# Kernel optimization log

Hardware: AMD Instinct MI355X
Metric: run time of the kernel (lower is better)

Reference implementation:

```python
import jax, jax.numpy as jnp
import numpy as np

B, C, CE, H, W = 4, 128, 64, 64, 64
V = H * W
# parent(i) < i//2 guarantees depth <= ceil(log2(V)) = 12; 14 is a safe static bound
MAX_LEVELS = 14


def _gather_v(x, idx):
    # x: [B, C, V], idx: [B, V] -> gather along vertex dim (broadcast over C)
    return jnp.take_along_axis(x, idx[:, None, :], axis=2)


def _tree_filter(feature_in, embed_in, sorted_index, sorted_parent, node_level):
    Bv, Cv, Hv, Wv = feature_in.shape
    Vv = Hv * Wv
    f = feature_in.reshape(Bv, Cv, Vv)
    e = embed_in.reshape(Bv, embed_in.shape[1], Vv)
    # build_edge_weight: gather to BFS order, gather parent, squared-L2 distance, exp(-d)
    f_s = _gather_v(f, sorted_index)          # [B,C,V] features in topological order
    e_s = _gather_v(e, sorted_index)
    e_p = _gather_v(e_s, sorted_parent)
    d2 = jnp.sum((e_s - e_p) ** 2, axis=1)    # [B,V]
    w = jnp.exp(-d2)                          # edge weight node->parent (root: exp(0)=1, unused)
    wB = w[:, None, :]
    # ---- up sweep (leaves -> root), level-parallel over BFS levels ----
    # A_i = f_i + sum_{c in child(i)} w_c * A_c ; Z_i = 1 + sum w_c * Z_c (self_weight = 1)
    aggr_up = f_s
    nrm_up = jnp.ones((Bv, Vv), feature_in.dtype)
    for d in range(MAX_LEVELS - 1, 0, -1):
        mw = jnp.where(node_level == d, w, jnp.zeros((), feature_in.dtype))
        aggr_up = jax.vmap(lambda a, p, m: a.at[:, p].add(m))(
            aggr_up, sorted_parent, mw[:, None, :] * aggr_up)
        nrm_up = jax.vmap(lambda a, p, m: a.at[p].add(m))(
            nrm_up, sorted_parent, mw * nrm_up)
    # ---- down sweep (root -> leaves) ----
    # Ahat_i = A_i + w_i * (Ahat_parent - w_i * A_i); root keeps A_root
    aggr = aggr_up
    nrm = nrm_up
    for d in range(1, MAX_LEVELS):
        sel = node_level == d
        pa = _gather_v(aggr, sorted_parent)
        aggr = jnp.where(sel[:, None, :], aggr_up + wB * (pa - wB * aggr_up), aggr)
        pn = jnp.take_along_axis(nrm, sorted_parent, axis=1)
        nrm = jnp.where(sel, nrm_up + w * (pn - w * nrm_up), nrm)
    out_s = aggr / nrm[:, None, :]
    # scatter back from BFS order to original vertex order
    out = jax.vmap(lambda o, i: jnp.zeros_like(o).at[:, i].set(o))(out_s, sorted_index)
    return out.reshape(Bv, Cv, Hv, Wv)


def setup_inputs() -> dict:
    key = jax.random.key(0)
    k1, k2 = jax.random.split(key)
    feature_in = jax.random.normal(k1, (B, C, H, W), dtype=jnp.float32)
    embed_in = 0.1 * jax.random.normal(k2, (B, CE, H, W), dtype=jnp.float32)
    rng = np.random.default_rng(0)
    sorted_index = np.stack([rng.permutation(V) for _ in range(B)]).astype(np.int32)
    sorted_parent = np.zeros((B, V), dtype=np.int32)
    node_level = np.zeros((B, V), dtype=np.int32)
    for b in range(B):
        for i in range(1, V):
            p = int(rng.integers(0, max(1, i // 2)))  # parent earlier in order, depth <= log2(V)
            sorted_parent[b, i] = p
            node_level[b, i] = node_level[b, p] + 1
    return {
        "feature_in": feature_in,
        "embed_in": embed_in,
        "sorted_index": jnp.asarray(sorted_index),
        "sorted_parent": jnp.asarray(sorted_parent),
        "node_level": jnp.asarray(node_level),
    }


def reference(feature_in, embed_in, sorted_index, sorted_parent, node_level):
    return _tree_filter(feature_in, embed_in, sorted_index, sorted_parent, node_level)
```

## Files before the change

### kernel.cpp

```cpp
#include <hip/hip_runtime.h>

#define BB 4
#define CC 128
#define CE 64
#define VV 4096
#define NLEV 14


__device__ __forceinline__ void lds_fadd(float* p, float v) {
    unsafeAtomicAdd(p, v);
}

__global__ __launch_bounds__(256) void prep_kernel(
    const float* __restrict__ embed,
    const int* __restrict__ sorted_index,
    const int* __restrict__ sorted_parent,
    const int* __restrict__ node_level,
    float* __restrict__ wsort,
    int*   __restrict__ giInv,
    int2*  __restrict__ cpl,
    int*   __restrict__ offs)
{
    int tid = threadIdx.x;
    if (blockIdx.x < BB) {
        int b = blockIdx.x;
        __shared__ int pos_s[VV];
        __shared__ int whist[4][16];
        __shared__ int cursor[NLEV];
        __shared__ int offSh[NLEV + 1];
        const int* lev = node_level    + b * VV;
        const int* si  = sorted_index  + b * VV;
        const int* par = sorted_parent + b * VV;
        int lane = tid & 63;
        int w    = tid >> 6;

        int dreg[16], sreg[16];
        int myc = 0;
        #pragma unroll
        for (int t = 0; t < 4; ++t) {
            int idx = tid + t * 256;
            int4 dv = ((const int4*)lev)[idx];
            int4 sv = ((const int4*)si)[idx];
            #pragma unroll
            for (int j = 0; j < 4; ++j) {
                int d = (&dv.x)[j]; d = d < NLEV - 1 ? d : NLEV - 1;
                dreg[t * 4 + j] = d;
                sreg[t * 4 + j] = (&sv.x)[j];
                #pragma unroll
                for (int dd = 0; dd < NLEV; ++dd) {
                    unsigned long long m = __ballot(d == dd);
                    myc += (lane == dd) ? (int)__popcll(m) : 0;
                }
            }
        }
        if (lane < 16) whist[w][lane] = myc;
        __syncthreads();
        if (tid == 0) {
            int acc = 0;
            for (int d = 0; d < NLEV; ++d) {
                int h = whist[0][d] + whist[1][d] + whist[2][d] + whist[3][d];
                offSh[d] = acc; cursor[d] = acc; acc += h;
            }
            offSh[NLEV] = acc;
        }
        __syncthreads();
        if (tid <= NLEV) offs[b * 16 + tid] = offSh[tid];

        int kreg[16];
        #pragma unroll
        for (int t = 0; t < 4; ++t) {
            #pragma unroll
            for (int j = 0; j < 4; ++j) {
                int i = 4 * (tid + t * 256) + j;
                int d = dreg[t * 4 + j];
                int k = 0;
                #pragma unroll
                for (int dd = 0; dd < NLEV; ++dd) {
                    unsigned long long m = __ballot(d == dd);
                    if (m) {
                        int leader = (int)__ffsll((unsigned long long)m) - 1;
                        int base = 0;
                        if (lane == leader) base = atomicAdd(&cursor[dd], (int)__popcll(m));
                        base = __shfl(base, leader, 64);
                        if (d == dd) k = base + (int)__popcll(m & ((1ull << lane) - 1ull));
                    }
                }
                kreg[t * 4 + j] = k;
                pos_s[i] = k;
                giInv[b * VV + sreg[t * 4 + j]] = k;
            }
        }
        __syncthreads();

        #pragma unroll
        for (int t = 0; t < 4; ++t) {
            int idx = tid + t * 256;
            int4 pv = ((const int4*)par)[idx];
            #pragma unroll
            for (int j = 0; j < 4; ++j) {
                int i = 4 * idx + j;
                int p = (&pv.x)[j];
                cpl[b * VV + kreg[t * 4 + j]] = make_int2(pos_s[p], i);
            }
        }
    } else {
        __shared__ float part[4][64];
        int bb   = blockIdx.x - BB;
        int b    = bb >> 6;
        int n0   = (bb & 63) << 6;
        int lane = tid & 63;
        int w    = tid >> 6;
        int i    = n0 + lane;
        int vi = sorted_index[b * VV + i];
        int p  = sorted_parent[b * VV + i];
        int vp = sorted_index[b * VV + p];
        const float* eb = embed + (size_t)b * CE * VV;
        float acc = 0.f;
        #pragma unroll
        for (int r = 0; r < 16; ++r) {
            int ce = w * 16 + r;
            float d = eb[ce * VV + vi] - eb[ce * VV + vp];
            acc = fmaf(d, d, acc);
        }
        part[w][lane] = acc;
        __syncthreads();
        if (w == 0) {
            float d2 = part[0][lane] + part[1][lane] + part[2][lane] + part[3][lane];
            wsort[b * VV + i] = __expf(-d2);
        }
    }
}

__global__ __launch_bounds__(512) void tree2_kernel(
    const float* __restrict__ feat,
    const float* __restrict__ wsort,
    const int*  __restrict__ giInv,
    const int2* __restrict__ cpl,
    const int*  __restrict__ offs,
    float* __restrict__ out)
{
    __shared__ float val0[VV];
    __shared__ float val1[VV];
    __shared__ float nrm[VV];
    __shared__ int   cw[VV];
    __shared__ int   offS[16];
    int b   = blockIdx.x >> 6;
    int c0  = (blockIdx.x & 63) << 1;
    int tid = threadIdx.x;

    const int2*  cplB = cpl   + b * VV;
    const int*   ivB  = giInv + b * VV;
    const float* wsB  = wsort + b * VV;
    const float* f0   = feat + ((size_t)(b * CC + c0)) * VV;
    const float* f1   = f0 + VV;

    if (tid < 16) offS[tid] = offs[b * 16 + tid];

    #pragma unroll
    for (int t = 0; t < 8; ++t) {
        int k = tid + t * 512;
        int2 x = cplB[k];
        int wb = __float_as_int(wsB[x.y]);
        cw[k] = (wb & 0xFFFFF000) | x.x;
    }

    int4 kkR[2];
    #pragma unroll
    for (int t = 0; t < 2; ++t) {
        int idx = tid + t * 512;
        int4   kk = ((const int4*)ivB)[idx];
        float4 a  = ((const float4*)f0)[idx];
        float4 bq = ((const float4*)f1)[idx];
        kkR[t] = kk;
        val0[kk.x] = a.x;  val0[kk.y] = a.y;  val0[kk.z] = a.z;  val0[kk.w] = a.w;
        val1[kk.x] = bq.x; val1[kk.y] = bq.y; val1[kk.z] = bq.z; val1[kk.w] = bq.w;
        nrm[kk.x] = 1.f;   nrm[kk.y] = 1.f;   nrm[kk.z] = 1.f;   nrm[kk.w] = 1.f;
    }
    __syncthreads();

    for (int d = NLEV - 1; d >= 1; --d) {
        int s = offS[d], e = offS[d + 1];
        if (s == e) continue;
        for (int k = s + tid; k < e; k += 512) {
            int x = cw[k];
            float w = __int_as_float(x & 0xFFFFF000);
            int  cp = x & 0xFFF;
            lds_fadd(&val0[cp], w * val0[k]);
            lds_fadd(&val1[cp], w * val1[k]);
            lds_fadd(&nrm[cp],  w * nrm[k]);
        }
        __syncthreads();
    }

    for (int d = 1; d <= NLEV - 1; ++d) {
        int s = offS[d], e = offS[d + 1];
        if (s == e) continue;
        for (int k = s + tid; k < e; k += 512) {
            int x = cw[k];
            float w = __int_as_float(x & 0xFFFFF000);
            int  cp = x & 0xFFF;
            float u0 = val0[k], u1 = val1[k], un = nrm[k];
            val0[k] = fmaf(w, fmaf(-w, u0, val0[cp]), u0);
            val1[k] = fmaf(w, fmaf(-w, u1, val1[cp]), u1);
            nrm[k]  = fmaf(w, fmaf(-w, un, nrm[cp]),  un);
        }
        __syncthreads();
    }

    float* o0 = out + ((size_t)(b * CC + c0)) * VV;
    float* o1 = o0 + VV;
    #pragma unroll
    for (int t = 0; t < 2; ++t) {
        int idx = tid + t * 512;
        int4 kk = kkR[t];
        float i0 = __fdividef(1.f, nrm[kk.x]);
        float i1 = __fdividef(1.f, nrm[kk.y]);
        float i2 = __fdividef(1.f, nrm[kk.z]);
        float i3 = __fdividef(1.f, nrm[kk.w]);
        float4 r0, r1;
        r0.x = val0[kk.x] * i0; r0.y = val0[kk.y] * i1;
        r0.z = val0[kk.z] * i2; r0.w = val0[kk.w] * i3;
        r1.x = val1[kk.x] * i0; r1.y = val1[kk.y] * i1;
        r1.z = val1[kk.z] * i2; r1.w = val1[kk.w] * i3;
        ((float4*)o0)[idx] = r0;
        ((float4*)o1)[idx] = r1;
    }
}

extern "C" void kernel_launch(void* const* d_in, const int* in_sizes, int n_in,
                              void* d_out, int out_size, void* d_ws, size_t ws_size,
                              hipStream_t stream) {
    const float* feat          = (const float*)d_in[0];
    const float* embed         = (const float*)d_in[1];
    const int*   sorted_index  = (const int*)d_in[2];
    const int*   sorted_parent = (const int*)d_in[3];
    const int*   node_level    = (const int*)d_in[4];
    float* out = (float*)d_out;

    char* ws = (char*)d_ws;
    const size_t A = (size_t)BB * VV * 4;
    float* wsort = (float*)(ws);
    int*   giInv = (int*)  (ws + A);
    int2*  cpl   = (int2*) (ws + 2 * A);
    int*   offs  = (int*)  (ws + 4 * A);

    prep_kernel<<<BB + BB * 64, 256, 0, stream>>>(
        embed, sorted_index, sorted_parent, node_level, wsort, giInv, cpl, offs);

    tree2_kernel<<<BB * CC / 2, 512, 0, stream>>>(
        feat, wsort, giInv, cpl, offs, out);
}
```

Baseline: 124.0 us.

## Replace ballot-based level bucketing with per-thread counts and LDS prefix scan

The per-batch sort of nodes by BFS level in the prep kernel now gives each thread a contiguous block of 16 vertices. Each thread counts and ranks them locally, and a shuffle-based exclusive scan over per-thread counts per level produces stable offsets. This replaces 14-way ballot loops and LDS atomics per element, cutting instruction count in the serial bucketing block. It adds a 14x256 int LDS table and changes global access to contiguous per-thread loads, which coalesce less well.

```diff
diff --git a/kernel.cpp b/kernel.cpp
--- a/kernel.cpp
+++ b/kernel.cpp
@@ -24,10 +24,11 @@
     int tid = threadIdx.x;
     if (blockIdx.x < BB) {
         int b = blockIdx.x;
-        __shared__ int pos_s[VV];
-        __shared__ int whist[4][16];
-        __shared__ int cursor[NLEV];
-        __shared__ int offSh[NLEV + 1];
+        __shared__ int  pos_s[VV];
+        __shared__ int4 cntv[NLEV * 64];
+        __shared__ int  tot[NLEV];
+        __shared__ int  offSh[NLEV + 1];
+        int* cnt = (int*)cntv;
         const int* lev = node_level    + b * VV;
         const int* si  = sorted_index  + b * VV;
         const int* par = sorted_parent + b * VV;
@@ -35,32 +36,59 @@
         int w    = tid >> 6;
 
         int dreg[16], sreg[16];
-        int myc = 0;
         #pragma unroll
         for (int t = 0; t < 4; ++t) {
-            int idx = tid + t * 256;
-            int4 dv = ((const int4*)lev)[idx];
-            int4 sv = ((const int4*)si)[idx];
+            int4 dv = ((const int4*)lev)[tid * 4 + t];
+            int4 sv = ((const int4*)si)[tid * 4 + t];
             #pragma unroll
             for (int j = 0; j < 4; ++j) {
                 int d = (&dv.x)[j]; d = d < NLEV - 1 ? d : NLEV - 1;
                 dreg[t * 4 + j] = d;
                 sreg[t * 4 + j] = (&sv.x)[j];
-                #pragma unroll
-                for (int dd = 0; dd < NLEV; ++dd) {
-                    unsigned long long m = __ballot(d == dd);
-                    myc += (lane == dd) ? (int)__popcll(m) : 0;
-                }
             }
         }
-        if (lane < 16) whist[w][lane] = myc;
+
+        int rank[16];
+        #pragma unroll
+        for (int m = 0; m < 16; ++m) {
+            int r = 0;
+            #pragma unroll
+            for (int m2 = 0; m2 < m; ++m2) r += (dreg[m2] == dreg[m]) ? 1 : 0;
+            rank[m] = r;
+        }
+
+        #pragma unroll
+        for (int d = 0; d < NLEV; ++d) {
+            int c = 0;
+            #pragma unroll
+            for (int m = 0; m < 16; ++m) c += (dreg[m] == d) ? 1 : 0;
+            cnt[d * 256 + tid] = c;
+        }
+        __syncthreads();
+
+        for (int d = w; d < NLEV; d += 4) {
+            int base = d * 64 + lane;
+            int4 cv = cntv[base];
+            int ls = cv.x + cv.y + cv.z + cv.w;
+            int x = ls;
+            #pragma unroll
+            for (int off = 1; off < 64; off <<= 1) {
+                int y = __shfl_up(x, off, 64);
+                if (lane >= off) x += y;
+            }
+            int excl = x - ls;
+            int4 ov;
+            ov.x = excl;
+            ov.y = excl + cv.x;
+            ov.z = excl + cv.x + cv.y;
+            ov.w = excl + cv.x + cv.y + cv.z;
+            cntv[base] = ov;
+            if (lane == 63) tot[d] = x;
+        }
         __syncthreads();
         if (tid == 0) {
             int acc = 0;
-            for (int d = 0; d < NLEV; ++d) {
-                int h = whist[0][d] + whist[1][d] + whist[2][d] + whist[3][d];
-                offSh[d] = acc; cursor[d] = acc; acc += h;
-            }
+            for (int d = 0; d < NLEV; ++d) { offSh[d] = acc; acc += tot[d]; }
             offSh[NLEV] = acc;
         }
         __syncthreads();
@@ -68,39 +96,23 @@
 
         int kreg[16];
         #pragma unroll
+        for (int m = 0; m < 16; ++m) {
+            int d = dreg[m];
+            int k = offSh[d] + cnt[d * 256 + tid] + rank[m];
+            kreg[m] = k;
+            pos_s[16 * tid + m] = k;
+            giInv[b * VV + sreg[m]] = k;
+        }
+        __syncthreads();
+
+        #pragma unroll
         for (int t = 0; t < 4; ++t) {
+            int4 pv = ((const int4*)par)[tid * 4 + t];
             #pragma unroll
             for (int j = 0; j < 4; ++j) {
-                int i = 4 * (tid + t * 256) + j;
-                int d = dreg[t * 4 + j];
-                int k = 0;
-                #pragma unroll
-                for (int dd = 0; dd < NLEV; ++dd) {
-                    unsigned long long m = __ballot(d == dd);
-                    if (m) {
-                        int leader = (int)__ffsll((unsigned long long)m) - 1;
-                        int base = 0;
-                        if (lane == leader) base = atomicAdd(&cursor[dd], (int)__popcll(m));
-                        base = __shfl(base, leader, 64);
-                        if (d == dd) k = base + (int)__popcll(m & ((1ull << lane) - 1ull));
-                    }
-                }
-                kreg[t * 4 + j] = k;
-                pos_s[i] = k;
-                giInv[b * VV + sreg[t * 4 + j]] = k;
-            }
-        }
-        __syncthreads();
-
-        #pragma unroll
-        for (int t = 0; t < 4; ++t) {
-            int idx = tid + t * 256;
-            int4 pv = ((const int4*)par)[idx];
-            #pragma unroll
-            for (int j = 0; j < 4; ++j) {
-                int i = 4 * idx + j;
+                int m = t * 4 + j;
                 int p = (&pv.x)[j];
-                cpl[b * VV + kreg[t * 4 + j]] = make_int2(pos_s[p], i);
+                cpl[b * VV + kreg[m]] = make_int2(pos_s[p], 16 * tid + m);
             }
         }
     } else {
```

New measurement: 103.3 us. -16.7%, faster.
